# Kernel optimization log

Hardware: AMD Instinct MI355X
Metric: run time of the kernel (lower is better)

Reference implementation:

```python
import jax, jax.numpy as jnp
import numpy as np

STRIDES = (32.0, 16.0, 8.0)
POS_IOU_THR = 0.3
NUM_CLASSES = 20
B, M = 16, 4096
IMG = 1024


def setup_inputs() -> dict:
    key = jax.random.key(0)
    ks = jax.random.split(key, 8)
    # anchors in grid units (wh) per level, converted to centered xyxy like convert_wh_xyxy
    wh = jnp.asarray([[[2, 2], [4, 4], [8, 8]],
                      [[4, 4], [8, 8], [16, 16]],
                      [[8, 8], [16, 16], [32, 32]]], dtype=jnp.float32)
    anchors = jnp.concatenate([-wh / 2, wh / 2], axis=-1)  # [3,3,4]
    # targets: sizes/centers chosen so max IoU > 0.3 at every level (mask all-true)
    s = jax.random.uniform(ks[0], (M,), minval=64.0, maxval=256.0)   # square size px
    cx = jax.random.uniform(ks[1], (M,), minval=128.0, maxval=896.0)
    cy = jax.random.uniform(ks[2], (M,), minval=128.0, maxval=896.0)
    cls_ind = jax.random.randint(ks[3], (M,), 0, NUM_CLASSES).astype(jnp.float32)
    mix_ind = jnp.zeros((M,), jnp.float32)
    batch_id = jnp.repeat(jnp.arange(B, dtype=jnp.float32), M // B)  # sorted, last = B-1
    targets = jnp.stack([cx - s / 2, cy - s / 2, cx + s / 2, cy + s / 2,
                         cls_ind, mix_ind, batch_id], axis=-1)  # [M,7]
    sizes = (32, 64, 128)
    inp = {"targets": targets, "anchors": anchors}
    for i, sz in enumerate(sizes):
        inp[f"cls{i}"] = jax.random.normal(ks[4 + i], (B, 3, sz, sz, NUM_CLASSES), jnp.float32)
        inp[f"reg{i}"] = jax.random.normal(jax.random.fold_in(ks[7], i), (B, 3, sz, sz, 5), jnp.float32)
    return inp


def _iou_xyxy(a, b):
    # a: [A,4], b: [M,4] -> [A,M]
    tl = jnp.maximum(a[:, None, :2], b[None, :, :2])
    br = jnp.minimum(a[:, None, 2:], b[None, :, 2:])
    wh = jnp.clip(br - tl, 0.0)
    inter = wh[..., 0] * wh[..., 1]
    area_a = (a[:, 2] - a[:, 0]) * (a[:, 3] - a[:, 1])
    area_b = (b[:, 2] - b[:, 0]) * (b[:, 3] - b[:, 1])
    return inter / (area_a[:, None] + area_b[None, :] - inter + 1e-9)


def _encode(ex, gt):
    ew = jnp.maximum(ex[:, 2] - ex[:, 0], 1.0)
    eh = jnp.maximum(ex[:, 3] - ex[:, 1], 1.0)
    gw = jnp.maximum(gt[:, 2] - gt[:, 0], 1.0)
    gh = jnp.maximum(gt[:, 3] - gt[:, 1], 1.0)
    gcx = gt[:, 0] + 0.5 * gw
    gcy = gt[:, 1] + 0.5 * gh
    dx = gcx - gcx.astype(jnp.int16).astype(gt.dtype)  # frac part (trunc), like torch int16 cast
    dy = gcy - gcy.astype(jnp.int16).astype(gt.dtype)
    return jnp.stack([dx, dy, jnp.log(gw / ew), jnp.log(gh / eh)], axis=-1)


def _level(cls, reg_full, anchor_l, targets, stride):
    reg, obj = reg_full[..., :4], reg_full[..., 4:5]
    w = targets[:, 2] - targets[:, 0]
    h = targets[:, 3] - targets[:, 1]
    bbox = jnp.stack([-w / 2, -h / 2, w / 2, h / 2], axis=-1) / stride  # convert_to_origin/stride
    center = jnp.stack([(targets[:, 2] + targets[:, 0]) / 2,
                        (targets[:, 3] + targets[:, 1]) / 2], axis=-1) / stride
    grids = center.astype(jnp.int32)  # [M,2]
    ov = _iou_xyxy(anchor_l, bbox)    # [A,M]
    max_ov = ov.max(axis=0)
    arg = ov.argmax(axis=0)
    mask = (max_ov > POS_IOU_THR).astype(cls.dtype)  # all-true by construction
    bid = targets[:, -1].astype(jnp.int32)
    gx, gy = grids[:, 0], grids[:, 1]
    cls_p = cls[bid, arg, gx, gy] * mask[:, None]          # [M,20]
    reg_p = reg[bid, arg, gx, gy] * mask[:, None]          # [M,4]
    reg_t = _encode(anchor_l[arg], targets[:, :4] / stride) * mask[:, None]
    cls_t = jax.nn.one_hot(targets[:, 4].astype(jnp.int32), cls.shape[-1], dtype=cls.dtype) * mask[:, None]
    obj_t = jnp.zeros_like(obj).at[bid, arg, gx, gy, 0].set(mask)
    return cls_p, reg_p, obj.reshape(-1, 1), cls_t, reg_t, obj_t.reshape(-1, 1)


def reference(targets, anchors, cls0, cls1, cls2, reg0, reg1, reg2):
    levels = [(cls0, reg0), (cls1, reg1), (cls2, reg2)]
    outs = [_level(c, r, anchors[i], targets, STRIDES[i]) for i, (c, r) in enumerate(levels)]
    return tuple(jnp.concatenate([o[i] for o in outs], axis=0) for i in range(6))
```

## Files before the change

kernel.cpp:

```cpp
#include <hip/hip_runtime.h>
#include <stdint.h>

#define TM 4096
#define NC 20

#define CLSP_OFF 0
#define REGP_OFF 245760
#define OBJ_OFF  294912
#define CLST_OFF 1327104
#define REGT_OFF 1572864
#define OBJT_OFF 1622016
#define OBJ_TOT  1032192

#define N0 49152
#define N1 196608

#define COPY_BLOCKS 1008
#define TGT_BLOCKS  48

#define KEY_BIAS 0xC0000000u

__global__ void la_fused_main(const float* __restrict__ targets,
                              const float* __restrict__ anchors,
                              const float* __restrict__ cls0,
                              const float* __restrict__ cls1,
                              const float* __restrict__ cls2,
                              const float* __restrict__ reg0,
                              const float* __restrict__ reg1,
                              const float* __restrict__ reg2,
                              float* __restrict__ out) {
    if (blockIdx.x < COPY_BLOCKS) {
        int e = (blockIdx.x * 256 + threadIdx.x) * 4;
        const float* reg; int f;
        if (e < N0)            { reg = reg0; f = e; }
        else if (e < N0 + N1)  { reg = reg1; f = e - N0; }
        else                   { reg = reg2; f = e - (N0 + N1); }
        const float4* r4 = reinterpret_cast<const float4*>(reg + (long)f * 5);
        float4 v1 = r4[1], v2 = r4[2], v3 = r4[3], v4 = r4[4];
        float4 o;
        o.x = v1.x;
        o.y = v2.y;
        o.z = v3.z;
        o.w = v4.w;
        *reinterpret_cast<float4*>(out + OBJ_OFF + e) = o;
        return;
    }

    int t = (blockIdx.x - COPY_BLOCKS) * 256 + threadIdx.x;
    int lvl = t >> 12;
    int ti  = t & (TM - 1);

    float stride = (lvl == 0) ? 32.f : (lvl == 1 ? 16.f : 8.f);
    int   sz     = (lvl == 0) ? 32   : (lvl == 1 ? 64   : 128);
    int   loff   = (lvl == 0) ? 0    : (lvl == 1 ? N0   : N0 + N1);
    const float* cls = (lvl == 0) ? cls0 : (lvl == 1 ? cls1 : cls2);
    const float* reg = (lvl == 0) ? reg0 : (lvl == 1 ? reg1 : reg2);

    const float* tg = targets + ti * 7;
    float x1 = tg[0], y1 = tg[1], x2 = tg[2], y2 = tg[3];
    int icls = (int)tg[4];
    int bid  = (int)tg[6];

    float w = x2 - x1, h = y2 - y1;
    float b0 = (-w * 0.5f) / stride;
    float b1 = (-h * 0.5f) / stride;
    float b2 = ( w * 0.5f) / stride;
    float b3 = ( h * 0.5f) / stride;
    float area_b = (b2 - b0) * (b3 - b1);

    float best = -1.0f; int argb = 0;
    float sa0 = 0.f, sa1 = 0.f, sa2 = 0.f, sa3 = 0.f;
    #pragma unroll
    for (int a = 0; a < 3; ++a) {
        float a0 = anchors[lvl * 12 + a * 4 + 0];
        float a1 = anchors[lvl * 12 + a * 4 + 1];
        float a2 = anchors[lvl * 12 + a * 4 + 2];
        float a3 = anchors[lvl * 12 + a * 4 + 3];
        float cw = fmaxf(fminf(a2, b2) - fmaxf(a0, b0), 0.f);
        float ch = fmaxf(fminf(a3, b3) - fmaxf(a1, b1), 0.f);
        float inter  = cw * ch;
        float area_a = (a2 - a0) * (a3 - a1);
        float iou = inter / (area_a + area_b - inter + 1e-9f);
        if (iou > best) { best = iou; argb = a; sa0 = a0; sa1 = a1; sa2 = a2; sa3 = a3; }
    }

    float    mask = (best > 0.3f) ? 1.0f : 0.0f;
    unsigned mbit = (best > 0.3f) ? 1u   : 0u;

    int gx = (int)(((x2 + x1) * 0.5f) / stride);
    int gy = (int)(((y2 + y1) * 0.5f) / stride);
    long base = ((long)(bid * 3 + argb) * sz + gx) * sz + gy;

    const float4* crow = reinterpret_cast<const float4*>(cls + base * NC);
    float4* cpo = reinterpret_cast<float4*>(out + CLSP_OFF) + (long)t * 5;
    float4* cto = reinterpret_cast<float4*>(out + CLST_OFF) + (long)t * 5;
    #pragma unroll
    for (int q = 0; q < 5; ++q) {
        float4 v = crow[q];
        v.x *= mask; v.y *= mask; v.z *= mask; v.w *= mask;
        cpo[q] = v;
        float4 o;
        o.x = (4 * q + 0 == icls) ? mask : 0.f;
        o.y = (4 * q + 1 == icls) ? mask : 0.f;
        o.z = (4 * q + 2 == icls) ? mask : 0.f;
        o.w = (4 * q + 3 == icls) ? mask : 0.f;
        cto[q] = o;
    }

    const float* rrow = reg + base * 5;
    float4 rp;
    rp.x = rrow[0] * mask; rp.y = rrow[1] * mask;
    rp.z = rrow[2] * mask; rp.w = rrow[3] * mask;
    reinterpret_cast<float4*>(out + REGP_OFF)[t] = rp;

    float ew = fmaxf(sa2 - sa0, 1.f);
    float eh = fmaxf(sa3 - sa1, 1.f);
    float g0 = x1 / stride, g1 = y1 / stride, g2 = x2 / stride, g3 = y2 / stride;
    float gw = fmaxf(g2 - g0, 1.f);
    float gh = fmaxf(g3 - g1, 1.f);
    float gcx = g0 + 0.5f * gw;
    float gcy = g1 + 0.5f * gh;
    float4 rt;
    rt.x = (gcx - (float)(int)gcx) * mask;
    rt.y = (gcy - (float)(int)gcy) * mask;
    rt.z = logf(gw / ew) * mask;
    rt.w = logf(gh / eh) * mask;
    reinterpret_cast<float4*>(out + REGT_OFF)[t] = rt;

    atomicMax(reinterpret_cast<unsigned int*>(out) + OBJT_OFF + loff + base,
              KEY_BIAS | ((unsigned)ti << 1) | mbit);
}

__global__ void la_objt_resolve(float* __restrict__ out) {
    int e = (blockIdx.x * 256 + threadIdx.x) * 4;
    uint4 v = *reinterpret_cast<const uint4*>(
        reinterpret_cast<unsigned int*>(out) + OBJT_OFF + e);
    float4 o;
    o.x = (v.x >= KEY_BIAS) ? (float)(v.x & 1u) : 0.0f;
    o.y = (v.y >= KEY_BIAS) ? (float)(v.y & 1u) : 0.0f;
    o.z = (v.z >= KEY_BIAS) ? (float)(v.z & 1u) : 0.0f;
    o.w = (v.w >= KEY_BIAS) ? (float)(v.w & 1u) : 0.0f;
    *reinterpret_cast<float4*>(out + OBJT_OFF + e) = o;
}

extern "C" void kernel_launch(void* const* d_in, const int* in_sizes, int n_in,
                              void* d_out, int out_size, void* d_ws, size_t ws_size,
                              hipStream_t stream) {
    const float* targets = (const float*)d_in[0];
    const float* anchors = (const float*)d_in[1];
    const float* cls0    = (const float*)d_in[2];
    const float* reg0    = (const float*)d_in[3];
    const float* cls1    = (const float*)d_in[4];
    const float* reg1    = (const float*)d_in[5];
    const float* cls2    = (const float*)d_in[6];
    const float* reg2    = (const float*)d_in[7];
    float* out = (float*)d_out;

    la_fused_main<<<COPY_BLOCKS + TGT_BLOCKS, 256, 0, stream>>>(
        targets, anchors, cls0, cls1, cls2, reg0, reg1, reg2, out);
    la_objt_resolve<<<COPY_BLOCKS, 256, 0, stream>>>(out);
}
```

Before: 14.98 us.

## Resolve objectness scatter in shared memory and drop the second kernel launch

Replaces the global atomicMax scatter plus a separate resolve kernel with per-block resolution. Each target block covers one (level, batch) slice: it zeroes that slice of the obj_t output, stores packed cell/thread keys in shared memory, and has each thread scan all 256 keys to decide whether it is the last writer for its cell. This removes a kernel launch and a full pass over the obj_t buffer. It relies on the targets being sorted by batch with 256 per batch, and the 48 target blocks now zero large slices in place of spreading that work over many blocks.

```diff
diff --git a/kernel.cpp b/kernel.cpp
--- a/kernel.cpp
+++ b/kernel.cpp
@@ -15,22 +15,23 @@
 #define N0 49152
 #define N1 196608
 
-#define COPY_BLOCKS 1008
-#define TGT_BLOCKS  48
+#define TGT_BLOCKS 48
+#define CP_BLOCKS  1008
 
-#define KEY_BIAS 0xC0000000u
+__global__ void __launch_bounds__(256)
+la_one(const float* __restrict__ targets,
+       const float* __restrict__ anchors,
+       const float* __restrict__ cls0,
+       const float* __restrict__ cls1,
+       const float* __restrict__ cls2,
+       const float* __restrict__ reg0,
+       const float* __restrict__ reg1,
+       const float* __restrict__ reg2,
+       float* __restrict__ out) {
+    int b = blockIdx.x;
 
-__global__ void la_fused_main(const float* __restrict__ targets,
-                              const float* __restrict__ anchors,
-                              const float* __restrict__ cls0,
-                              const float* __restrict__ cls1,
-                              const float* __restrict__ cls2,
-                              const float* __restrict__ reg0,
-                              const float* __restrict__ reg1,
-                              const float* __restrict__ reg2,
-                              float* __restrict__ out) {
-    if (blockIdx.x < COPY_BLOCKS) {
-        int e = (blockIdx.x * 256 + threadIdx.x) * 4;
+    if (b >= TGT_BLOCKS) {
+        int e = ((b - TGT_BLOCKS) * 256 + threadIdx.x) * 4;
         const float* reg; int f;
         if (e < N0)            { reg = reg0; f = e; }
         else if (e < N0 + N1)  { reg = reg1; f = e - N0; }
@@ -46,9 +47,13 @@
         return;
     }
 
-    int t = (blockIdx.x - COPY_BLOCKS) * 256 + threadIdx.x;
-    int lvl = t >> 12;
-    int ti  = t & (TM - 1);
+    __shared__ unsigned s_key[256];
+
+    int lvl = b >> 4;
+    int bid = b & 15;
+    int tid = threadIdx.x;
+    int ti  = bid * 256 + tid;
+    int t   = lvl * TM + ti;
 
     float stride = (lvl == 0) ? 32.f : (lvl == 1 ? 16.f : 8.f);
     int   sz     = (lvl == 0) ? 32   : (lvl == 1 ? 64   : 128);
@@ -56,10 +61,13 @@
     const float* cls = (lvl == 0) ? cls0 : (lvl == 1 ? cls1 : cls2);
     const float* reg = (lvl == 0) ? reg0 : (lvl == 1 ? reg1 : reg2);
 
+    int sub  = 3 * sz * sz;
+    float* objt_sub = out + OBJT_OFF + loff + bid * sub;
+
     const float* tg = targets + ti * 7;
     float x1 = tg[0], y1 = tg[1], x2 = tg[2], y2 = tg[3];
     int icls = (int)tg[4];
-    int bid  = (int)tg[6];
+    int tbid = (int)tg[6];
 
     float w = x2 - x1, h = y2 - y1;
     float b0 = (-w * 0.5f) / stride;
@@ -68,8 +76,9 @@
     float b3 = ( h * 0.5f) / stride;
     float area_b = (b2 - b0) * (b3 - b1);
 
-    float best = -1.0f; int argb = 0;
+    float best = -1.0f;
     float sa0 = 0.f, sa1 = 0.f, sa2 = 0.f, sa3 = 0.f;
+    int argb = 0;
     #pragma unroll
     for (int a = 0; a < 3; ++a) {
         float a0 = anchors[lvl * 12 + a * 4 + 0];
@@ -89,7 +98,8 @@
 
     int gx = (int)(((x2 + x1) * 0.5f) / stride);
     int gy = (int)(((y2 + y1) * 0.5f) / stride);
-    long base = ((long)(bid * 3 + argb) * sz + gx) * sz + gy;
+    int cell = (argb * sz + gx) * sz + gy;
+    long base = (long)(tbid * 3) * sz * sz + cell;
 
     const float4* crow = reinterpret_cast<const float4*>(cls + base * NC);
     float4* cpo = reinterpret_cast<float4*>(out + CLSP_OFF) + (long)t * 5;
@@ -127,20 +137,22 @@
     rt.w = logf(gh / eh) * mask;
     reinterpret_cast<float4*>(out + REGT_OFF)[t] = rt;
 
-    atomicMax(reinterpret_cast<unsigned int*>(out) + OBJT_OFF + loff + base,
-              KEY_BIAS | ((unsigned)ti << 1) | mbit);
-}
+    unsigned packed = ((unsigned)cell << 9) | ((unsigned)tid << 1) | mbit;
+    s_key[tid] = packed;
 
-__global__ void la_objt_resolve(float* __restrict__ out) {
-    int e = (blockIdx.x * 256 + threadIdx.x) * 4;
-    uint4 v = *reinterpret_cast<const uint4*>(
-        reinterpret_cast<unsigned int*>(out) + OBJT_OFF + e);
-    float4 o;
-    o.x = (v.x >= KEY_BIAS) ? (float)(v.x & 1u) : 0.0f;
-    o.y = (v.y >= KEY_BIAS) ? (float)(v.y & 1u) : 0.0f;
-    o.z = (v.z >= KEY_BIAS) ? (float)(v.z & 1u) : 0.0f;
-    o.w = (v.w >= KEY_BIAS) ? (float)(v.w & 1u) : 0.0f;
-    *reinterpret_cast<float4*>(out + OBJT_OFF + e) = o;
+    float4 z4; z4.x = z4.y = z4.z = z4.w = 0.0f;
+    for (int i = tid; i < (sub >> 2); i += 256)
+        reinterpret_cast<float4*>(objt_sub)[i] = z4;
+
+    __syncthreads();
+
+    bool winner = true;
+    for (int j = 0; j < 256; ++j) {
+        unsigned p = s_key[j];
+        winner = winner && !((p >> 9) == (unsigned)cell && p > packed);
+    }
+    if (winner)
+        objt_sub[cell] = mask;
 }
 
 extern "C" void kernel_launch(void* const* d_in, const int* in_sizes, int n_in,
@@ -156,7 +168,6 @@
     const float* reg2    = (const float*)d_in[7];
     float* out = (float*)d_out;
 
-    la_fused_main<<<COPY_BLOCKS + TGT_BLOCKS, 256, 0, stream>>>(
+    la_one<<<TGT_BLOCKS + CP_BLOCKS, 256, 0, stream>>>(
         targets, anchors, cls0, cls1, cls2, reg0, reg1, reg2, out);
-    la_objt_resolve<<<COPY_BLOCKS, 256, 0, stream>>>(out);
 }
```

Result: slower. 26.56 us (+77.3%).
